# Optimization experiments

Hardware: AMD Instinct MI355X
Metric: run time of the kernel (lower is better)

The kernel has to match this reference:

```python
import jax, jax.numpy as jnp
import numpy as np

B, D, T = 16384, 1024, 128  # batch, embed_dim, num_degradation_types
V, L = 4, 3                 # variants per sample, degradations per variant


def setup_inputs() -> dict:
    key = jax.random.key(0)
    k1, k2, k3, k4 = jax.random.split(key, 4)
    clean_embeddings = jax.random.normal(k1, (B, D), dtype=jnp.float32)
    W = jax.random.normal(k2, (T, D), dtype=jnp.float32) * (1.0 / np.sqrt(D))
    b = jnp.zeros((T,), dtype=jnp.float32)
    deg_indices = jax.random.randint(k3, (B, V, L), 0, T, dtype=jnp.int32)
    deg_mask = jax.random.randint(k4, (B, V, L), 0, 2, dtype=jnp.int32)
    return {"clean_embeddings": clean_embeddings, "W": W, "b": b,
            "deg_indices": deg_indices, "deg_mask": deg_mask}


def reference(clean_embeddings, W, b, deg_indices, deg_mask):
    # Linear + softmax: [B, T]
    logits = jnp.einsum("bd,td->bt", clean_embeddings, W) + b
    probs = jax.nn.softmax(logits, axis=-1)
    # Gather probs at each (batch, label) pair: [B, V*L] -> [B, V, L]
    flat_idx = deg_indices.reshape(B, V * L)
    gathered = jnp.take_along_axis(probs, flat_idx, axis=1).reshape(B, V, L)
    # Masked sum over all labels of a sample, divided by max(num_variants, 1)=V
    per_sample = (gathered * deg_mask.astype(probs.dtype)).sum(axis=(1, 2)) / V
    return per_sample.sum() / B
```

## Files before the change

kernel.cpp:

```cpp
#include <hip/hip_runtime.h>

#define B_SIZE 16384
#define D_DIM  1024
#define T_DIM  128
#define VLn    12
#define BM     32
#define BK     64
#define NCHUNK (D_DIM / BK)
#define GRID   (B_SIZE / BM)
#define SL_STRIDE 132

typedef _Float16 half8  __attribute__((ext_vector_type(8)));
typedef __fp16   fp16x2 __attribute__((ext_vector_type(2)));
typedef float    f32x4  __attribute__((ext_vector_type(4)));

union Pack16 { fp16x2 h[4]; uint4 u; };

__device__ __forceinline__ uint4 pack8(float4 v0, float4 v1) {
    Pack16 un;
    un.h[0] = __builtin_amdgcn_cvt_pkrtz(v0.x, v0.y);
    un.h[1] = __builtin_amdgcn_cvt_pkrtz(v0.z, v0.w);
    un.h[2] = __builtin_amdgcn_cvt_pkrtz(v1.x, v1.y);
    un.h[3] = __builtin_amdgcn_cvt_pkrtz(v1.z, v1.w);
    return un.u;
}

__global__ __launch_bounds__(256)
void conv_w(const float* __restrict__ W, uint4* __restrict__ Wf) {
    const int j    = blockIdx.x * 256 + threadIdx.x;
    const int kc   = j >> 10;
    const int r    = j & 1023;
    const int g    = r >> 6;
    const int lane = r & 63;
    const int ks = g >> 3, CT = g & 7;
    const int n = CT * 16 + (lane & 15);
    const int k = kc * 64 + ks * 32 + ((lane >> 4) << 3);
    const float* src = W + (size_t)n * D_DIM + k;
    const float4 v0 = *(const float4*)src;
    const float4 v1 = *(const float4*)(src + 4);
    Wf[j] = pack8(v0, v1);
}

__global__ __launch_bounds__(256, 2)
void qloss_kernel(const float* __restrict__ emb,
                  const uint4* __restrict__ Wf,
                  const float* __restrict__ bias,
                  const int*   __restrict__ didx,
                  const int*   __restrict__ dmsk,
                  float*       __restrict__ part)
{
    __shared__ __align__(16) unsigned char smem[40960 + 32];
    float* sL   = (float*)smem;
    float* sRed = (float*)(smem + 40960);

    const int t    = threadIdx.x;
    const int w    = t >> 6;
    const int lane = t & 63;
    const int m15  = lane & 15;
    const int quad = lane >> 4;
    const int r0   = blockIdx.x * BM;

    const int sg   = t >> 6, sl = t & 63;
    const int srow = (sg >> 1) * 16 + (sl & 15);
    const int skk  = (sg & 1) * 32 + ((sl >> 4) << 3);
    const float* aBase = emb + (size_t)(r0 + srow) * D_DIM + skk;

    f32x4 acc[2][2];
#pragma unroll
    for (int mt = 0; mt < 2; ++mt)
#pragma unroll
        for (int ct = 0; ct < 2; ++ct) acc[mt][ct] = (f32x4){0.f, 0.f, 0.f, 0.f};

    {
        const float4 v0 = *(const float4*)(aBase);
        const float4 v1 = *(const float4*)(aBase + 4);
        *(uint4*)(smem + t * 16) = pack8(v0, v1);
#pragma unroll
        for (int p = 0; p < 4; ++p) {
            const int u = t + p * 256;
            *(uint4*)(smem + 8192 + u * 16) = Wf[u];
        }
    }
    __syncthreads();

    for (int kc = 0; kc < NCHUNK; ++kc) {
        const int cur = kc & 1;
        unsigned char* sAc = smem + cur * 4096;
        unsigned char* sWc = smem + 8192 + cur * 16384;
        unsigned char* sAn = smem + (cur ^ 1) * 4096;
        unsigned char* sWn = smem + 8192 + (cur ^ 1) * 16384;

        float4 v0, v1; uint4 wv[4];
        if (kc + 1 < NCHUNK) {
            v0 = *(const float4*)(aBase + (kc + 1) * 64);
            v1 = *(const float4*)(aBase + (kc + 1) * 64 + 4);
#pragma unroll
            for (int p = 0; p < 4; ++p)
                wv[p] = Wf[(size_t)(kc + 1) * 1024 + t + p * 256];
        }

#pragma unroll
        for (int ks = 0; ks < 2; ++ks) {
            const half8 a0 = *(const half8*)(sAc + ((0 * 2 + ks) * 64 + lane) * 16);
            const half8 a1 = *(const half8*)(sAc + ((1 * 2 + ks) * 64 + lane) * 16);
            const half8 b0 = *(const half8*)(sWc + ((ks * 8 + w * 2 + 0) * 64 + lane) * 16);
            const half8 b1 = *(const half8*)(sWc + ((ks * 8 + w * 2 + 1) * 64 + lane) * 16);
            acc[0][0] = __builtin_amdgcn_mfma_f32_16x16x32_f16(a0, b0, acc[0][0], 0, 0, 0);
            acc[0][1] = __builtin_amdgcn_mfma_f32_16x16x32_f16(a0, b1, acc[0][1], 0, 0, 0);
            acc[1][0] = __builtin_amdgcn_mfma_f32_16x16x32_f16(a1, b0, acc[1][0], 0, 0, 0);
            acc[1][1] = __builtin_amdgcn_mfma_f32_16x16x32_f16(a1, b1, acc[1][1], 0, 0, 0);
        }

        if (kc + 1 < NCHUNK) {
            *(uint4*)(sAn + t * 16) = pack8(v0, v1);
#pragma unroll
            for (int p = 0; p < 4; ++p) {
                const int u = t + p * 256;
                *(uint4*)(sWn + u * 16) = wv[p];
            }
        }
        __syncthreads();
    }

    const int CT0 = w * 2;
    const float b0v = bias[CT0 * 16 + m15];
    const float b1v = bias[(CT0 + 1) * 16 + m15];
#pragma unroll
    for (int mt = 0; mt < 2; ++mt)
#pragma unroll
        for (int i = 0; i < 4; ++i) {
            const int row = mt * 16 + quad * 4 + i;
            sL[row * SL_STRIDE + CT0 * 16 + m15]       = acc[mt][0][i] + b0v;
            sL[row * SL_STRIDE + (CT0 + 1) * 16 + m15] = acc[mt][1][i] + b1v;
        }
    __syncthreads();

    {
        const int row = t >> 3, s = t & 7;
        float* base = &sL[row * SL_STRIDE + s * 16];
        float v[16];
#pragma unroll
        for (int j = 0; j < 4; ++j) *(float4*)&v[j * 4] = *(const float4*)(base + j * 4);
        float m = -1e30f;
#pragma unroll
        for (int j = 0; j < 16; ++j) m = fmaxf(m, v[j]);
#pragma unroll
        for (int off = 1; off < 8; off <<= 1) m = fmaxf(m, __shfl_xor(m, off));
        float ssum = 0.f;
#pragma unroll
        for (int j = 0; j < 16; ++j) { v[j] = __expf(v[j] - m); ssum += v[j]; }
#pragma unroll
        for (int off = 1; off < 8; off <<= 1) ssum += __shfl_xor(ssum, off);
        const float inv = 1.0f / ssum;
#pragma unroll
        for (int j = 0; j < 16; ++j) v[j] *= inv;
#pragma unroll
        for (int j = 0; j < 4; ++j) *(float4*)(base + j * 4) = *(const float4*)&v[j * 4];
    }
    __syncthreads();

    float p = 0.f;
#pragma unroll
    for (int i = t; i < BM * VLn; i += 256) {
        const int gi  = r0 * VLn + i;
        const int row = i / VLn;
        const int idx = didx[gi];
        const int mk  = dmsk[gi];
        p += mk ? sL[row * SL_STRIDE + idx] : 0.f;
    }
#pragma unroll
    for (int off = 1; off < 64; off <<= 1) p += __shfl_xor(p, off);
    if (lane == 0) sRed[w] = p;
    __syncthreads();
    if (t == 0) part[blockIdx.x] = sRed[0] + sRed[1] + sRed[2] + sRed[3];
}

__global__ __launch_bounds__(256)
void reduce_k(const float* __restrict__ part, float* __restrict__ out) {
    __shared__ float s[4];
    const int t = threadIdx.x;
    float p = part[t] + part[t + 256];
#pragma unroll
    for (int off = 1; off < 64; off <<= 1) p += __shfl_xor(p, off);
    if ((t & 63) == 0) s[t >> 6] = p;
    __syncthreads();
    if (t == 0) out[0] = (s[0] + s[1] + s[2] + s[3]) * (1.0f / 65536.0f);
}

extern "C" void kernel_launch(void* const* d_in, const int* in_sizes, int n_in,
                              void* d_out, int out_size, void* d_ws, size_t ws_size,
                              hipStream_t stream) {
    const float* emb  = (const float*)d_in[0];
    const float* W    = (const float*)d_in[1];
    const float* bias = (const float*)d_in[2];
    const int*   didx = (const int*)d_in[3];
    const int*   dmsk = (const int*)d_in[4];
    float* out = (float*)d_out;

    uint4* Wf   = (uint4*)d_ws;
    float* part = (float*)((char*)d_ws + 262144);

    conv_w<<<64, 256, 0, stream>>>(W, Wf);
    qloss_kernel<<<GRID, 256, 0, stream>>>(emb, Wf, bias, didx, dmsk, part);
    reduce_k<<<1, 256, 0, stream>>>(part, out);
}
```

Baseline: 116.5 us.

## Load W fragments directly into registers with two-deep prefetch, shrink LDS

Each wave now loads its own pre-swizzled fp16 W fragments straight from global memory into registers, using a three-stage register pipeline (current, next, next+1), instead of staging all of W through double-buffered shared memory. Shared memory drops to the A double buffer plus the logits tile, and the launch bound is raised to 4 blocks per SM to improve occupancy. The change also fully unrolls the K loop. The trade-off is that the W fragments are fetched redundantly from L2 by each block, and register pressure is higher.

```diff
diff --git a/kernel.cpp b/kernel.cpp
--- a/kernel.cpp
+++ b/kernel.cpp
@@ -15,6 +15,7 @@
 typedef float    f32x4  __attribute__((ext_vector_type(4)));
 
 union Pack16 { fp16x2 h[4]; uint4 u; };
+union BReg   { uint4 u; half8 h; };
 
 __device__ __forceinline__ uint4 pack8(float4 v0, float4 v1) {
     Pack16 un;
@@ -41,7 +42,7 @@
     Wf[j] = pack8(v0, v1);
 }
 
-__global__ __launch_bounds__(256, 2)
+__global__ __launch_bounds__(256, 4)
 void qloss_kernel(const float* __restrict__ emb,
                   const uint4* __restrict__ Wf,
                   const float* __restrict__ bias,
@@ -49,9 +50,9 @@
                   const int*   __restrict__ dmsk,
                   float*       __restrict__ part)
 {
-    __shared__ __align__(16) unsigned char smem[40960 + 32];
+    __shared__ __align__(16) unsigned char smem[16928];
     float* sL   = (float*)smem;
-    float* sRed = (float*)(smem + 40960);
+    float* sRed = (float*)(smem + 16896);
 
     const int t    = threadIdx.x;
     const int w    = t >> 6;
@@ -65,60 +66,62 @@
     const int skk  = (sg & 1) * 32 + ((sl >> 4) << 3);
     const float* aBase = emb + (size_t)(r0 + srow) * D_DIM + skk;
 
+    const uint4* wBase = Wf + (size_t)(2 * w) * 64 + lane;
+
     f32x4 acc[2][2];
 #pragma unroll
     for (int mt = 0; mt < 2; ++mt)
 #pragma unroll
         for (int ct = 0; ct < 2; ++ct) acc[mt][ct] = (f32x4){0.f, 0.f, 0.f, 0.f};
 
+    BReg bcur[4], bnx1[4], bnx2[4];
     {
         const float4 v0 = *(const float4*)(aBase);
         const float4 v1 = *(const float4*)(aBase + 4);
         *(uint4*)(smem + t * 16) = pack8(v0, v1);
 #pragma unroll
-        for (int p = 0; p < 4; ++p) {
-            const int u = t + p * 256;
-            *(uint4*)(smem + 8192 + u * 16) = Wf[u];
-        }
-    }
-    __syncthreads();
-
+        for (int ks = 0; ks < 2; ++ks)
+#pragma unroll
+            for (int j = 0; j < 2; ++j) {
+                bcur[ks * 2 + j].u = wBase[(size_t)(ks * 8 + j) * 64];
+                bnx1[ks * 2 + j].u = wBase[(size_t)1 * 1024 + (ks * 8 + j) * 64];
+            }
+    }
+    __syncthreads();
+
+#pragma unroll
     for (int kc = 0; kc < NCHUNK; ++kc) {
-        const int cur = kc & 1;
-        unsigned char* sAc = smem + cur * 4096;
-        unsigned char* sWc = smem + 8192 + cur * 16384;
-        unsigned char* sAn = smem + (cur ^ 1) * 4096;
-        unsigned char* sWn = smem + 8192 + (cur ^ 1) * 16384;
-
-        float4 v0, v1; uint4 wv[4];
+        unsigned char* sAc = smem + (kc & 1) * 4096;
+        unsigned char* sAn = smem + ((kc & 1) ^ 1) * 4096;
+
+        float4 va0, va1;
         if (kc + 1 < NCHUNK) {
-            v0 = *(const float4*)(aBase + (kc + 1) * 64);
-            v1 = *(const float4*)(aBase + (kc + 1) * 64 + 4);
-#pragma unroll
-            for (int p = 0; p < 4; ++p)
-                wv[p] = Wf[(size_t)(kc + 1) * 1024 + t + p * 256];
+            va0 = *(const float4*)(aBase + (kc + 1) * 64);
+            va1 = *(const float4*)(aBase + (kc + 1) * 64 + 4);
+        }
+        if (kc + 2 < NCHUNK) {
+#pragma unroll
+            for (int ks = 0; ks < 2; ++ks)
+#pragma unroll
+                for (int j = 0; j < 2; ++j)
+                    bnx2[ks * 2 + j].u =
+                        wBase[(size_t)(kc + 2) * 1024 + (ks * 8 + j) * 64];
         }
 
 #pragma unroll
         for (int ks = 0; ks < 2; ++ks) {
             const half8 a0 = *(const half8*)(sAc + ((0 * 2 + ks) * 64 + lane) * 16);
             const half8 a1 = *(const half8*)(sAc + ((1 * 2 + ks) * 64 + lane) * 16);
-            const half8 b0 = *(const half8*)(sWc + ((ks * 8 + w * 2 + 0) * 64 + lane) * 16);
-            const half8 b1 = *(const half8*)(sWc + ((ks * 8 + w * 2 + 1) * 64 + lane) * 16);
-            acc[0][0] = __builtin_amdgcn_mfma_f32_16x16x32_f16(a0, b0, acc[0][0], 0, 0, 0);
-            acc[0][1] = __builtin_amdgcn_mfma_f32_16x16x32_f16(a0, b1, acc[0][1], 0, 0, 0);
-            acc[1][0] = __builtin_amdgcn_mfma_f32_16x16x32_f16(a1, b0, acc[1][0], 0, 0, 0);
-            acc[1][1] = __builtin_amdgcn_mfma_f32_16x16x32_f16(a1, b1, acc[1][1], 0, 0, 0);
-        }
-
-        if (kc + 1 < NCHUNK) {
-            *(uint4*)(sAn + t * 16) = pack8(v0, v1);
-#pragma unroll
-            for (int p = 0; p < 4; ++p) {
-                const int u = t + p * 256;
-                *(uint4*)(sWn + u * 16) = wv[p];
-            }
-        }
+            acc[0][0] = __builtin_amdgcn_mfma_f32_16x16x32_f16(a0, bcur[ks * 2 + 0].h, acc[0][0], 0, 0, 0);
+            acc[0][1] = __builtin_amdgcn_mfma_f32_16x16x32_f16(a0, bcur[ks * 2 + 1].h, acc[0][1], 0, 0, 0);
+            acc[1][0] = __builtin_amdgcn_mfma_f32_16x16x32_f16(a1, bcur[ks * 2 + 0].h, acc[1][0], 0, 0, 0);
+            acc[1][1] = __builtin_amdgcn_mfma_f32_16x16x32_f16(a1, bcur[ks * 2 + 1].h, acc[1][1], 0, 0, 0);
+        }
+
+        if (kc + 1 < NCHUNK)
+            *(uint4*)(sAn + t * 16) = pack8(va0, va1);
+#pragma unroll
+        for (int q = 0; q < 4; ++q) { bcur[q] = bnx1[q]; bnx1[q] = bnx2[q]; }
         __syncthreads();
     }
 
```

New measurement: 115.5 us. No clear change (-0.8%).
